# Kernel optimization log

Hardware: AMD Instinct MI355X
Metric: run time of the kernel (lower is better)

Reference implementation:

```python
import jax, jax.numpy as jnp
import numpy as np


def _frac_weights(b_d, k):
    # d = 0.5*sigmoid(b_d), per hidden unit; fractional-differencing coeffs
    # c_j = prod_{i=0}^{j-1} (i - d)/(i + 1), j = 1..k (c_1 = -d).
    # Returned ordered oldest-lag-first to match history buffer ordering.
    d = 0.5 * jax.nn.sigmoid(b_d[0])                      # (H,)
    i = jnp.arange(k, dtype=d.dtype)[:, None]             # (k,1)
    factors = (i - d[None, :]) / (i + 1.0)                # (k,H)
    coeff = jnp.cumprod(factors, axis=0)                  # coeff[j-1] = c_j
    return coeff[::-1]                                    # (k,H)


def setup_inputs() -> dict:
    key = jax.random.key(0)
    T, B, I, H, K, O = 128, 256, 512, 512, 32, 5
    ks = jax.random.split(key, 12)
    s_i = 1.0 / np.sqrt(I)
    s_h = 1.0 / np.sqrt(H)
    return {
        "inputs": jax.random.normal(ks[0], (T, B, I), jnp.float32),
        "length": jax.random.randint(ks[1], (B,), 0, T),
        "b_d": jnp.zeros((1, H), jnp.float32),
        # mLSTM cell (3 gates: input, output, candidate)
        "W_mih": jax.random.normal(ks[2], (3 * H, I), jnp.float32) * s_i,
        "W_mhh": jax.random.normal(ks[3], (3 * H, H), jnp.float32) * s_h,
        "b_mih": jax.random.normal(ks[4], (3 * H,), jnp.float32) * s_h,
        "b_mhh": jax.random.normal(ks[5], (3 * H,), jnp.float32) * s_h,
        # torch.nn.LSTMCell (4 gates: i, f, g, o)
        "W_ih": jax.random.normal(ks[6], (4 * H, H), jnp.float32) * s_h,
        "W_hh": jax.random.normal(ks[7], (4 * H, H), jnp.float32) * s_h,
        "b_ih": jax.random.normal(ks[8], (4 * H,), jnp.float32) * s_h,
        "b_hh": jax.random.normal(ks[9], (4 * H,), jnp.float32) * s_h,
        # hidden2output
        "W_out": jax.random.normal(ks[10], (O, H), jnp.float32) * s_h,
        "b_out": jax.random.normal(ks[11], (O,), jnp.float32) * s_h,
        "k": K,
    }


def reference(inputs, length, b_d, W_mih, W_mhh, b_mih, b_mhh,
              W_ih, W_hh, b_ih, b_hh, W_out, b_out, k):
    T, B, I = inputs.shape
    H = b_d.shape[1]
    wd = _frac_weights(b_d, k)                            # (k,H)

    def step(carry, x_t):
        h1, hist, h2, c2 = carry
        # --- mLSTM fixed-d cell ---
        g = x_t @ W_mih.T + b_mih + h1 @ W_mhh.T + b_mhh  # (B,3H)
        ig, og, gg = jnp.split(g, 3, axis=1)
        i_g, o_g, cand = jax.nn.sigmoid(ig), jax.nn.sigmoid(og), jnp.tanh(gg)
        # fractional-d long-memory filter over last k cell states
        c1 = i_g * cand - jnp.einsum('kh,kbh->bh', wd, hist)
        hist = jnp.concatenate([hist[1:], c1[None]], axis=0)
        h1n = o_g * jnp.tanh(c1)
        # --- standard LSTMCell on top ---
        g2 = h1n @ W_ih.T + b_ih + h2 @ W_hh.T + b_hh     # (B,4H)
        i2, f2, gc2, o2 = jnp.split(g2, 4, axis=1)
        c2n = jax.nn.sigmoid(f2) * c2 + jax.nn.sigmoid(i2) * jnp.tanh(gc2)
        h2n = jnp.tanh(jax.nn.sigmoid(o2) * jnp.tanh(c2n))  # extra tanh as in source
        return (h1n, hist, h2n, c2n), h2n

    z = jnp.zeros((B, H), inputs.dtype)
    init = (z, jnp.zeros((k, B, H), inputs.dtype), z, z)
    _, outs = jax.lax.scan(step, init, inputs)            # (T,B,H)
    sel = outs[length, jnp.arange(B)]                     # (B,H) gather per sample
    logit = sel @ W_out.T + b_out
    return jax.nn.log_softmax(logit, axis=1)
```

## Files before the change

### kernel.cpp

```cpp
#include <hip/hip_runtime.h>
#include <hip/hip_cooperative_groups.h>
#include <cstdint>
#include <cstddef>

typedef __attribute__((ext_vector_type(8))) short short8;
typedef __attribute__((ext_vector_type(4))) float floatx4;

#define T_STEPS 128
#define BATCH   256
#define IDIM    512
#define HDIM    512
#define KHIST   32
#define RDEPTH  16

#define WA_STRIDE 520
#define WB_STRIDE 1032
#define LDS_BYTES 148480

#define FSTR 32
#define POLL_SLEEP 8


__device__ __forceinline__ unsigned short f2bf(float x) {
  union { float f; unsigned u; } v; v.f = x;
  unsigned r = v.u + 0x7fffu + ((v.u >> 16) & 1u);
  return (unsigned short)(r >> 16);
}
__device__ __forceinline__ float bf2f(unsigned short s) {
  union { unsigned u; float f; } v; v.u = ((unsigned)s) << 16; return v.f;
}
__device__ __forceinline__ float sigm(float x) { return 1.0f / (1.0f + __expf(-x)); }
__device__ __forceinline__ float tanh_f(float x) {
  float ax = fabsf(x);
  float e = __expf(-2.0f * ax);
  float t = (1.0f - e) / (1.0f + e);
  return x < 0.0f ? -t : t;
}

__device__ __forceinline__ void llc_issue_16B(const unsigned short* p, short8* r) {
  asm volatile("global_load_dwordx4 %0, %1, off sc0 sc1"
               : "=v"(*r) : "v"(p) : "memory");
}
__device__ __forceinline__ void l2_issue_16B(const unsigned short* p, short8* r) {
  asm volatile("global_load_dwordx4 %0, %1, off sc0"
               : "=v"(*r) : "v"(p) : "memory");
}
__device__ __forceinline__ void llc_store_4rows32(unsigned short* p,
                                                  unsigned short a, unsigned short b,
                                                  unsigned short c, unsigned short d) {
  asm volatile(
    "global_store_short %4, %0, off sc0 sc1\n\t"
    "global_store_short %4, %1, off offset:32 sc0 sc1\n\t"
    "global_store_short %4, %2, off offset:64 sc0 sc1\n\t"
    "global_store_short %4, %3, off offset:96 sc0 sc1"
    :: "v"((unsigned)a), "v"((unsigned)b), "v"((unsigned)c), "v"((unsigned)d), "v"(p)
    : "memory");
}
__device__ __forceinline__ void l2_store_4rows32(unsigned short* p,
                                                 unsigned short a, unsigned short b,
                                                 unsigned short c, unsigned short d) {
  asm volatile(
    "global_store_short %4, %0, off sc0\n\t"
    "global_store_short %4, %1, off offset:32 sc0\n\t"
    "global_store_short %4, %2, off offset:64 sc0\n\t"
    "global_store_short %4, %3, off offset:96 sc0"
    :: "v"((unsigned)a), "v"((unsigned)b), "v"((unsigned)c), "v"((unsigned)d), "v"(p)
    : "memory");
}
__device__ __forceinline__ int flag_ld_llc(const int* p) {
  int v; asm volatile("global_load_dword %0, %1, off sc0 sc1\n\ts_waitcnt vmcnt(0)"
                      : "=v"(v) : "v"(p) : "memory"); return v;
}
__device__ __forceinline__ void flag_st_llc(int* p, int v) {
  asm volatile("global_store_dword %0, %1, off sc0 sc1" :: "v"(p), "v"(v) : "memory");
}
__device__ __forceinline__ void drain_vm() {
  asm volatile("s_waitcnt vmcnt(0)" ::: "memory");
}

#define PREP_BLOCKS 20016
__global__ __launch_bounds__(256) void prep_all(
    const float* __restrict__ x, const float* __restrict__ Wmih, const float* __restrict__ Wmhh,
    const float* __restrict__ Wih, const float* __restrict__ Whh,
    const float* __restrict__ b_d, const float* __restrict__ b_mih, const float* __restrict__ b_mhh,
    const float* __restrict__ b_ih, const float* __restrict__ b_hh,
    unsigned short* __restrict__ Xb, unsigned short* __restrict__ Wmih_b,
    unsigned short* __restrict__ Wmhh_b, unsigned short* __restrict__ W2,
    float* __restrict__ wd2, float* __restrict__ bA, float* __restrict__ bB,
    int* __restrict__ counters) {
  const int blk = blockIdx.x, tid = threadIdx.x;
  if (blk < 16384) {
    int i = blk * 256 + tid;
    float4 v = reinterpret_cast<const float4*>(x)[i];
    ushort4 o; o.x = f2bf(v.x); o.y = f2bf(v.y); o.z = f2bf(v.z); o.w = f2bf(v.w);
    reinterpret_cast<ushort4*>(Xb)[i] = o;
  } else if (blk < 17152) {
    int i = (blk - 16384) * 256 + tid;
    float4 v = reinterpret_cast<const float4*>(Wmih)[i];
    ushort4 o; o.x = f2bf(v.x); o.y = f2bf(v.y); o.z = f2bf(v.z); o.w = f2bf(v.w);
    reinterpret_cast<ushort4*>(Wmih_b)[i] = o;
  } else if (blk < 17920) {
    int i = (blk - 17152) * 256 + tid;
    float4 v = reinterpret_cast<const float4*>(Wmhh)[i];
    ushort4 o; o.x = f2bf(v.x); o.y = f2bf(v.y); o.z = f2bf(v.z); o.w = f2bf(v.w);
    reinterpret_cast<ushort4*>(Wmhh_b)[i] = o;
  } else if (blk < 19968) {
    int i4 = (blk - 17920) * 256 + tid;
    int i = i4 * 4; int n = i >> 10; int k = i & 1023;
    float4 v = (k < 512) ? reinterpret_cast<const float4*>(Wih + n * 512 + k)[0]
                         : reinterpret_cast<const float4*>(Whh + n * 512 + (k - 512))[0];
    ushort4 o; o.x = f2bf(v.x); o.y = f2bf(v.y); o.z = f2bf(v.z); o.w = f2bf(v.w);
    reinterpret_cast<ushort4*>(W2 + i)[0] = o;
  } else if (blk < 19984) {
    int t = (blk - 19968) * 256 + tid;
    if (t < 512) {
      float d = 0.5f * sigm(b_d[t]);
      float c = 1.0f;
      for (int i = 0; i < KHIST; ++i) {
        c *= ((float)i - d) / ((float)i + 1.0f);
        wd2[i * HDIM + t] = c;
      }
    } else if (t < 2048) {
      int n = t - 512;
      bA[n] = b_mih[n] + b_mhh[n];
    } else {
      int n = t - 2048;
      bB[n] = b_ih[n] + b_hh[n];
    }
  } else {
    int i = (blk - 19984) * 256 + tid;
    counters[i] = 0;
  }
}

__global__ __launch_bounds__(256) void gx_gemm_kernel(const unsigned short* __restrict__ Xb,
                                                      const unsigned short* __restrict__ Wb,
                                                      const float* __restrict__ bA,
                                                      unsigned short* __restrict__ GXh) {
  __shared__ unsigned short As[2][128 * 32];
  __shared__ unsigned short Bs[2][128 * 32];
  const int tid = threadIdx.x;
  const int lane = tid & 63;
  const int wv = tid >> 6;
  const int q = lane >> 4, r16 = lane & 15;
  const int wr = wv >> 1, wc = wv & 1;
  const int bid = (int)blockIdx.x;
  const int m0 = (bid & 255) * 128;
  const int n0 = (bid >> 8) * 128;

  const int sr0 = tid >> 2, sc0 = (tid & 3) * 8;
  const int sr1 = (256 + tid) >> 2, sc1 = (tid & 3) * 8;

  floatx4 acc[4][4];
  #pragma unroll
  for (int i = 0; i < 4; ++i)
    #pragma unroll
    for (int j = 0; j < 4; ++j) acc[i][j] = (floatx4){0.f, 0.f, 0.f, 0.f};

  {
    short8 a0 = *(const short8*)(Xb + (size_t)(m0 + sr0) * IDIM + sc0);
    short8 a1 = *(const short8*)(Xb + (size_t)(m0 + sr1) * IDIM + sc1);
    short8 b0 = *(const short8*)(Wb + (size_t)(n0 + sr0) * IDIM + sc0);
    short8 b1 = *(const short8*)(Wb + (size_t)(n0 + sr1) * IDIM + sc1);
    *(short8*)(As[0] + sr0 * 32 + sc0) = a0;
    *(short8*)(As[0] + sr1 * 32 + sc1) = a1;
    *(short8*)(Bs[0] + sr0 * 32 + sc0) = b0;
    *(short8*)(Bs[0] + sr1 * 32 + sc1) = b1;
  }

  for (int t = 0; t < 16; ++t) {
    const int cur = t & 1;
    __syncthreads();
    short8 a0, a1, b0, b1;
    if (t < 15) {
      int k0 = (t + 1) * 32;
      a0 = *(const short8*)(Xb + (size_t)(m0 + sr0) * IDIM + k0 + sc0);
      a1 = *(const short8*)(Xb + (size_t)(m0 + sr1) * IDIM + k0 + sc1);
      b0 = *(const short8*)(Wb + (size_t)(n0 + sr0) * IDIM + k0 + sc0);
      b1 = *(const short8*)(Wb + (size_t)(n0 + sr1) * IDIM + k0 + sc1);
    }
    short8 af[4], bf[4];
    #pragma unroll
    for (int i = 0; i < 4; ++i)
      af[i] = *(const short8*)(As[cur] + (wr * 64 + i * 16 + r16) * 32 + q * 8);
    #pragma unroll
    for (int j = 0; j < 4; ++j)
      bf[j] = *(const short8*)(Bs[cur] + (wc * 64 + j * 16 + r16) * 32 + q * 8);
    #pragma unroll
    for (int i = 0; i < 4; ++i)
      #pragma unroll
      for (int j = 0; j < 4; ++j)
        acc[i][j] = __builtin_amdgcn_mfma_f32_16x16x32_bf16(af[i], bf[j], acc[i][j], 0, 0, 0);
    if (t < 15) {
      *(short8*)(As[cur ^ 1] + sr0 * 32 + sc0) = a0;
      *(short8*)(As[cur ^ 1] + sr1 * 32 + sc1) = a1;
      *(short8*)(Bs[cur ^ 1] + sr0 * 32 + sc0) = b0;
      *(short8*)(Bs[cur ^ 1] + sr1 * 32 + sc1) = b1;
    }
  }

  #pragma unroll
  for (int j = 0; j < 4; ++j) {
    int col = n0 + wc * 64 + j * 16 + r16;
    float bias = bA[col];
    #pragma unroll
    for (int i = 0; i < 4; ++i) {
      #pragma unroll
      for (int jj = 0; jj < 4; ++jj) {
        int row = m0 + wr * 64 + i * 16 + q * 4 + jj;
        GXh[(size_t)row * 1536 + col] = f2bf(acc[i][j][jj] + bias);
      }
    }
  }
}

__global__ __launch_bounds__(512, 1) void recurrent2(
    const unsigned short* __restrict__ GXh,
    const unsigned short* __restrict__ Wmhh,
    const unsigned short* __restrict__ W2,
    const float* __restrict__ bB,
    const float* __restrict__ wd2,
    unsigned short* __restrict__ h1L2,
    unsigned short* __restrict__ h1LLC,
    unsigned short* __restrict__ h2his,
    float* __restrict__ sel,
    const int* __restrict__ length,
    int* __restrict__ counters) {
  extern __shared__ char lds[];
  const int tid = threadIdx.x;
  const int lane = tid & 63;
  const int wv = tid >> 6;
  const int q = lane >> 4, r16 = lane & 15;
  const int xcd = (int)blockIdx.x & 7;
  const int bs = xcd >> 1;
  const bool isA = (xcd & 1) == 0;
  const int hs = (int)blockIdx.x >> 3;
  const int hcol = hs * 16 + r16;
  int* aFlags = counters + bs * 1024;
  int* bFlags = counters + 4096 + bs * 1024;

  if (isA) {
    unsigned short* WA = (unsigned short*)lds;
    unsigned short* HI = (unsigned short*)(lds + 48 * WA_STRIDE * 2);
    for (int idx = tid; idx < 48 * 64; idx += 512) {
      int rowi = idx >> 6, kc = idx & 63;
      int g = rowi >> 4, c = rowi & 15;
      const unsigned short* src = Wmhh + ((size_t)(g * 512 + hs * 16 + c)) * 512 + kc * 8;
      *(short8*)(WA + rowi * WA_STRIDE + kc * 8) = *(const short8*)src;
    }
    for (int idx = tid; idx < 4096; idx += 512)
      ((uint4*)HI)[idx] = (uint4){0, 0, 0, 0};
    float wdr[KHIST];
    #pragma unroll
    for (int l = 0; l < KHIST; ++l) wdr[l] = wd2[l * HDIM + hcol];
    __syncthreads();

    const int mi = wv & 3;
    const int m0 = bs * 64 + mi * 16;
    const int rg = mi * 4 + q;

    for (int s = 0; s < T_STEPS; ++s) {
      unsigned short gu[12];
      if (wv < 4) {
        #pragma unroll
        for (int j = 0; j < 4; ++j) {
          int row = m0 + q * 4 + j;
          size_t gidx = ((size_t)s * BATCH + row) * 1536 + hcol;
          gu[j]     = GXh[gidx];
          gu[4 + j] = GXh[gidx + 512];
          gu[8 + j] = GXh[gidx + 1024];
        }
      }
      if (wv < 4) {
        if (s > 0 && lane < 32) {
          const int* f = aFlags + lane * FSTR;
          while (flag_ld_llc(f) < s) __builtin_amdgcn_s_sleep(POLL_SLEEP);
        }
      } else if (wv == 4) {
        int tgt = s - (RDEPTH - 1);
        if (tgt > 0 && lane < 32) {
          const int* f = bFlags + lane * FSTR;
          while (flag_ld_llc(f) < tgt) __builtin_amdgcn_s_sleep(POLL_SLEEP);
        }
      }
      float c1[4];
      unsigned short h1w[4];
      if (wv < 4) {
        short8 af[16];
        if (s > 0) {
          const unsigned short* ab = h1L2 +
              (((size_t)((s - 1) & 15) * 4 + bs) << 15) +
              (size_t)(mi * 16 + r16) * 16 + (q & 1) * 8 + (q >> 1) * 1024;
          #pragma unroll
          for (int kk = 0; kk < 16; ++kk)
            l2_issue_16B(ab + (size_t)kk * 2048, &af[kk]);
        }
        float f0 = 0.f, f1 = 0.f, f2 = 0.f, f3 = 0.f;
        #pragma unroll
        for (int jj = 1; jj <= KHIST; ++jj) {
          int sl = (s - jj) & (KHIST - 1);
          ushort4 hv = *(const ushort4*)(HI + ((size_t)(sl * 16 + rg) * 16 + r16) * 4);
          float wc = wdr[jj - 1];
          f0 += wc * bf2f(hv.x); f1 += wc * bf2f(hv.y);
          f2 += wc * bf2f(hv.z); f3 += wc * bf2f(hv.w);
        }
        float fj[4] = {f0, f1, f2, f3};
        floatx4 acc[3];
        #pragma unroll
        for (int g = 0; g < 3; ++g) acc[g] = (floatx4){0.f, 0.f, 0.f, 0.f};
        if (s > 0) {
          drain_vm();
          __builtin_amdgcn_sched_barrier(0);
          #pragma unroll
          for (int kk = 0; kk < 16; ++kk) {
            #pragma unroll
            for (int g = 0; g < 3; ++g) {
              short8 b = *(const short8*)(WA + (size_t)(g * 16 + r16) * WA_STRIDE + kk * 32 + q * 8);
              acc[g] = __builtin_amdgcn_mfma_f32_16x16x32_bf16(af[kk], b, acc[g], 0, 0, 0);
            }
          }
        }
        #pragma unroll
        for (int j = 0; j < 4; ++j) {
          float gI = bf2f(gu[j])     + acc[0][j];
          float gO = bf2f(gu[4 + j]) + acc[1][j];
          float gG = bf2f(gu[8 + j]) + acc[2][j];
          float ig = sigm(gI), og = sigm(gO), cd = tanh_f(gG);
          float c1v = ig * cd - fj[j];
          c1[j] = c1v;
          h1w[j] = f2bf(og * tanh_f(c1v));
        }
      }
      __syncthreads();
      if (wv < 4) {
        size_t hoff = (((size_t)(s & 15) * 4 + bs) << 15) + (size_t)hs * 1024 +
                      (size_t)(mi * 16 + q * 4) * 16 + r16;
        l2_store_4rows32(h1L2 + hoff, h1w[0], h1w[1], h1w[2], h1w[3]);
        llc_store_4rows32(h1LLC + hoff, h1w[0], h1w[1], h1w[2], h1w[3]);
        ushort4 hw;
        hw.x = f2bf(c1[0]); hw.y = f2bf(c1[1]); hw.z = f2bf(c1[2]); hw.w = f2bf(c1[3]);
        *(ushort4*)(HI + ((size_t)((s & (KHIST - 1)) * 16 + rg) * 16 + r16) * 4) = hw;
      }
      drain_vm();
      __syncthreads();
      if (tid == 0)
        flag_st_llc(aFlags + hs * FSTR, s + 1);
    }
  } else {
    unsigned short* WB = (unsigned short*)lds;
    float* EX = (float*)(lds + 64 * WB_STRIDE * 2);
    for (int idx = tid; idx < 64 * 128; idx += 512) {
      int rowi = idx >> 7, kc = idx & 127;
      int g = rowi >> 4, c = rowi & 15;
      const unsigned short* src = W2 + ((size_t)(g * 512 + hs * 16 + c)) * 1024 + kc * 8;
      *(short8*)(WB + rowi * WB_STRIDE + kc * 8) = *(const short8*)src;
    }
    const int mi = wv >> 1, kh = wv & 1;
    const int m0 = bs * 64 + mi * 16;
    float c2r[4] = {0.f, 0.f, 0.f, 0.f};
    int lenr[4];
    float bBr[4];
    #pragma unroll
    for (int j = 0; j < 4; ++j) lenr[j] = length[m0 + q * 4 + j];
    #pragma unroll
    for (int g = 0; g < 4; ++g) bBr[g] = bB[g * 512 + hcol];
    __syncthreads();

    for (int t = 0; t < T_STEPS; ++t) {
      if (kh == 0) {
        if (lane < 32) {
          const int* f = aFlags + lane * FSTR;
          while (flag_ld_llc(f) < t + 1) __builtin_amdgcn_s_sleep(POLL_SLEEP);
        }
      } else {
        if (t > 0 && lane < 32) {
          const int* f = bFlags + lane * FSTR;
          while (flag_ld_llc(f) < t) __builtin_amdgcn_s_sleep(POLL_SLEEP);
        }
      }
      floatx4 acc[4];
      #pragma unroll
      for (int g = 0; g < 4; ++g) acc[g] = (floatx4){0.f, 0.f, 0.f, 0.f};
      bool doit = !(kh == 1 && t == 0);
      if (doit) {
        short8 af[16];
        const size_t lrow = (size_t)(mi * 16 + r16) * 16 + (q & 1) * 8 + (q >> 1) * 1024;
        if (kh == 0) {
          const unsigned short* ab = h1LLC + (((size_t)(t & 15) * 4 + bs) << 15) + lrow;
          #pragma unroll
          for (int kk = 0; kk < 16; ++kk)
            llc_issue_16B(ab + (size_t)kk * 2048, &af[kk]);
        } else {
          const unsigned short* ab = h2his + (((size_t)((t - 1) & 15) * 4 + bs) << 15) + lrow;
          #pragma unroll
          for (int kk = 0; kk < 16; ++kk)
            l2_issue_16B(ab + (size_t)kk * 2048, &af[kk]);
        }
        drain_vm();
        __builtin_amdgcn_sched_barrier(0);
        #pragma unroll
        for (int kk = 0; kk < 16; ++kk) {
          #pragma unroll
          for (int g = 0; g < 4; ++g) {
            short8 b = *(const short8*)(WB + (size_t)(g * 16 + r16) * WB_STRIDE + kh * 512 + kk * 32 + q * 8);
            acc[g] = __builtin_amdgcn_mfma_f32_16x16x32_bf16(af[kk], b, acc[g], 0, 0, 0);
          }
        }
      }
      if (kh == 1) {
        #pragma unroll
        for (int g = 0; g < 4; ++g)
          *(floatx4*)(EX + ((size_t)(mi * 4 + g) * 64 + lane) * 4) = acc[g];
      }
      __syncthreads();
      if (kh == 0) {
        #pragma unroll
        for (int g = 0; g < 4; ++g)
          acc[g] += *(const floatx4*)(EX + ((size_t)(mi * 4 + g) * 64 + lane) * 4);
        unsigned short h2w[4];
        #pragma unroll
        for (int j = 0; j < 4; ++j) {
          int row = m0 + q * 4 + j;
          float gi = acc[0][j] + bBr[0];
          float gf = acc[1][j] + bBr[1];
          float gg = acc[2][j] + bBr[2];
          float go = acc[3][j] + bBr[3];
          float c2n = sigm(gf) * c2r[j] + sigm(gi) * tanh_f(gg);
          c2r[j] = c2n;
          float h2n = tanh_f(sigm(go) * tanh_f(c2n));
          h2w[j] = f2bf(h2n);
          if (lenr[j] == t) sel[(size_t)row * 512 + hcol] = h2n;
        }
        size_t hoff = (((size_t)(t & 15) * 4 + bs) << 15) + (size_t)hs * 1024 +
                      (size_t)(mi * 16 + q * 4) * 16 + r16;
        l2_store_4rows32(h2his + hoff, h2w[0], h2w[1], h2w[2], h2w[3]);
      }
      drain_vm();
      __syncthreads();
      if (tid == 0)
        flag_st_llc(bFlags + hs * FSTR, t + 1);
    }
  }
}

__global__ void out_head_kernel(const float* __restrict__ sel, const float* __restrict__ Wout,
                                const float* __restrict__ bout, float* __restrict__ out) {
  int b = blockIdx.x, lane = threadIdx.x;
  float acc[5] = {0.f, 0.f, 0.f, 0.f, 0.f};
  for (int j = lane; j < HDIM; j += 64) {
    float x = sel[(size_t)b * HDIM + j];
    #pragma unroll
    for (int o = 0; o < 5; ++o) acc[o] += x * Wout[o * HDIM + j];
  }
  #pragma unroll
  for (int o = 0; o < 5; ++o)
    for (int off = 32; off > 0; off >>= 1) acc[o] += __shfl_down(acc[o], off);
  if (lane == 0) {
    float v[5]; float m = -1e30f;
    #pragma unroll
    for (int o = 0; o < 5; ++o) { v[o] = acc[o] + bout[o]; m = fmaxf(m, v[o]); }
    float s = 0.f;
    #pragma unroll
    for (int o = 0; o < 5; ++o) s += __expf(v[o] - m);
    float l = logf(s) + m;
    #pragma unroll
    for (int o = 0; o < 5; ++o) out[b * 5 + o] = v[o] - l;
  }
}

extern "C" void kernel_launch(void* const* d_in, const int* in_sizes, int n_in,
                              void* d_out, int out_size, void* d_ws, size_t ws_size,
                              hipStream_t stream) {
  const float* x      = (const float*)d_in[0];
  const int*   length = (const int*)d_in[1];
  const float* b_d    = (const float*)d_in[2];
  const float* W_mih  = (const float*)d_in[3];
  const float* W_mhh  = (const float*)d_in[4];
  const float* b_mih  = (const float*)d_in[5];
  const float* b_mhh  = (const float*)d_in[6];
  const float* W_ih   = (const float*)d_in[7];
  const float* W_hh   = (const float*)d_in[8];
  const float* b_ih   = (const float*)d_in[9];
  const float* b_hh   = (const float*)d_in[10];
  const float* W_out  = (const float*)d_in[11];
  const float* b_out  = (const float*)d_in[12];
  float* out = (float*)d_out;

  char* ws = (char*)d_ws;
  size_t off = 0;
  auto take = [&](size_t bytes) -> char* {
    char* p = ws + off;
    off += (bytes + 255) & ~(size_t)255;
    return p;
  };

  unsigned short* Xb     = (unsigned short*)take((size_t)T_STEPS * BATCH * IDIM * 2);
  unsigned short* Wmih_b = (unsigned short*)take(1536 * 512 * 2);
  unsigned short* Wmhh_b = (unsigned short*)take(1536 * 512 * 2);
  unsigned short* W2_b   = (unsigned short*)take(2048 * 1024 * 2);
  float* bA  = (float*)take(1536 * 4);
  float* bB  = (float*)take(2048 * 4);
  float* wd2 = (float*)take(KHIST * HDIM * 4);
  unsigned short* h1L2  = (unsigned short*)take((size_t)RDEPTH * BATCH * 512 * 2);
  unsigned short* h1LLC = (unsigned short*)take((size_t)RDEPTH * BATCH * 512 * 2);
  unsigned short* h2his = (unsigned short*)take((size_t)RDEPTH * BATCH * 512 * 2);
  float* sel = (float*)take((size_t)BATCH * HDIM * 4);
  int* counters = (int*)take(32768);
  unsigned short* GXh = (unsigned short*)take((size_t)T_STEPS * BATCH * 1536 * 2);
  if (off > ws_size) return;

  prep_all<<<PREP_BLOCKS, 256, 0, stream>>>(x, W_mih, W_mhh, W_ih, W_hh,
                                            b_d, b_mih, b_mhh, b_ih, b_hh,
                                            Xb, Wmih_b, Wmhh_b, W2_b, wd2, bA, bB, counters);
  gx_gemm_kernel<<<3072, 256, 0, stream>>>(Xb, Wmih_b, bA, GXh);

  hipFuncSetAttribute((const void*)recurrent2, hipFuncAttributeMaxDynamicSharedMemorySize, LDS_BYTES);
  void* kargs[] = { (void*)&GXh, (void*)&Wmhh_b, (void*)&W2_b, (void*)&bB, (void*)&wd2,
                    (void*)&h1L2, (void*)&h1LLC, (void*)&h2his, (void*)&sel, (void*)&length,
                    (void*)&counters };
  hipLaunchCooperativeKernel((void*)recurrent2, dim3(256), dim3(512), kargs, LDS_BYTES, stream);

  out_head_kernel<<<BATCH, 64, 0, stream>>>(sel, W_out, b_out, out);
}
```

Before: 1.008 ms.

## Defer LLC publish of h1 by one step and swap LSTM K-half roles

```diff
diff --git a/kernel.cpp b/kernel.cpp
--- a/kernel.cpp
+++ b/kernel.cpp
@@ -258,8 +258,12 @@
     const int mi = wv & 3;
     const int m0 = bs * 64 + mi * 16;
     const int rg = mi * 4 + q;
+    size_t dhoff = 0;
+    unsigned short dh1w[4] = {0, 0, 0, 0};
 
     for (int s = 0; s < T_STEPS; ++s) {
+      if (wv < 4 && s > 0)
+        llc_store_4rows32(h1LLC + dhoff, dh1w[0], dh1w[1], dh1w[2], dh1w[3]);
       unsigned short gu[12];
       if (wv < 4) {
         #pragma unroll
@@ -283,8 +287,6 @@
           while (flag_ld_llc(f) < tgt) __builtin_amdgcn_s_sleep(POLL_SLEEP);
         }
       }
-      float c1[4];
-      unsigned short h1w[4];
       if (wv < 4) {
         short8 af[16];
         if (s > 0) {
@@ -320,6 +322,8 @@
             }
           }
         }
+        float c1[4];
+        unsigned short h1w[4];
         #pragma unroll
         for (int j = 0; j < 4; ++j) {
           float gI = bf2f(gu[j])     + acc[0][j];
@@ -330,13 +334,12 @@
           c1[j] = c1v;
           h1w[j] = f2bf(og * tanh_f(c1v));
         }
-      }
-      __syncthreads();
-      if (wv < 4) {
         size_t hoff = (((size_t)(s & 15) * 4 + bs) << 15) + (size_t)hs * 1024 +
                       (size_t)(mi * 16 + q * 4) * 16 + r16;
         l2_store_4rows32(h1L2 + hoff, h1w[0], h1w[1], h1w[2], h1w[3]);
-        llc_store_4rows32(h1LLC + hoff, h1w[0], h1w[1], h1w[2], h1w[3]);
+        dhoff = hoff;
+        #pragma unroll
+        for (int j = 0; j < 4; ++j) dh1w[j] = h1w[j];
         ushort4 hw;
         hw.x = f2bf(c1[0]); hw.y = f2bf(c1[1]); hw.z = f2bf(c1[2]); hw.w = f2bf(c1[3]);
         *(ushort4*)(HI + ((size_t)((s & (KHIST - 1)) * 16 + rg) * 16 + r16) * 4) = hw;
@@ -346,6 +349,12 @@
       if (tid == 0)
         flag_st_llc(aFlags + hs * FSTR, s + 1);
     }
+    if (wv < 4)
+      llc_store_4rows32(h1LLC + dhoff, dh1w[0], dh1w[1], dh1w[2], dh1w[3]);
+    drain_vm();
+    __syncthreads();
+    if (tid == 0)
+      flag_st_llc(aFlags + hs * FSTR, T_STEPS + 1);
   } else {
     unsigned short* WB = (unsigned short*)lds;
     float* EX = (float*)(lds + 64 * WB_STRIDE * 2);
@@ -367,10 +376,10 @@
     __syncthreads();
 
     for (int t = 0; t < T_STEPS; ++t) {
-      if (kh == 0) {
+      if (kh == 1) {
         if (lane < 32) {
           const int* f = aFlags + lane * FSTR;
-          while (flag_ld_llc(f) < t + 1) __builtin_amdgcn_s_sleep(POLL_SLEEP);
+          while (flag_ld_llc(f) < t + 2) __builtin_amdgcn_s_sleep(POLL_SLEEP);
         }
       } else {
         if (t > 0 && lane < 32) {
@@ -381,36 +390,42 @@
       floatx4 acc[4];
       #pragma unroll
       for (int g = 0; g < 4; ++g) acc[g] = (floatx4){0.f, 0.f, 0.f, 0.f};
-      bool doit = !(kh == 1 && t == 0);
-      if (doit) {
+      const size_t lrow = (size_t)(mi * 16 + r16) * 16 + (q & 1) * 8 + (q >> 1) * 1024;
+      if (kh == 1) {
         short8 af[16];
-        const size_t lrow = (size_t)(mi * 16 + r16) * 16 + (q & 1) * 8 + (q >> 1) * 1024;
-        if (kh == 0) {
-          const unsigned short* ab = h1LLC + (((size_t)(t & 15) * 4 + bs) << 15) + lrow;
-          #pragma unroll
-          for (int kk = 0; kk < 16; ++kk)
-            llc_issue_16B(ab + (size_t)kk * 2048, &af[kk]);
-        } else {
-          const unsigned short* ab = h2his + (((size_t)((t - 1) & 15) * 4 + bs) << 15) + lrow;
-          #pragma unroll
-          for (int kk = 0; kk < 16; ++kk)
-            l2_issue_16B(ab + (size_t)kk * 2048, &af[kk]);
-        }
+        const unsigned short* ab = h1LLC + (((size_t)(t & 15) * 4 + bs) << 15) + lrow;
+        #pragma unroll
+        for (int kk = 0; kk < 16; ++kk)
+          llc_issue_16B(ab + (size_t)kk * 2048, &af[kk]);
         drain_vm();
         __builtin_amdgcn_sched_barrier(0);
         #pragma unroll
         for (int kk = 0; kk < 16; ++kk) {
           #pragma unroll
           for (int g = 0; g < 4; ++g) {
-            short8 b = *(const short8*)(WB + (size_t)(g * 16 + r16) * WB_STRIDE + kh * 512 + kk * 32 + q * 8);
+            short8 b = *(const short8*)(WB + (size_t)(g * 16 + r16) * WB_STRIDE + kk * 32 + q * 8);
             acc[g] = __builtin_amdgcn_mfma_f32_16x16x32_bf16(af[kk], b, acc[g], 0, 0, 0);
           }
         }
-      }
-      if (kh == 1) {
         #pragma unroll
         for (int g = 0; g < 4; ++g)
           *(floatx4*)(EX + ((size_t)(mi * 4 + g) * 64 + lane) * 4) = acc[g];
+      } else if (t > 0) {
+        short8 af[16];
+        const unsigned short* ab = h2his + (((size_t)((t - 1) & 15) * 4 + bs) << 15) + lrow;
+        #pragma unroll
+        for (int kk = 0; kk < 16; ++kk)
+          l2_issue_16B(ab + (size_t)kk * 2048, &af[kk]);
+        drain_vm();
+        __builtin_amdgcn_sched_barrier(0);
+        #pragma unroll
+        for (int kk = 0; kk < 16; ++kk) {
+          #pragma unroll
+          for (int g = 0; g < 4; ++g) {
+            short8 b = *(const short8*)(WB + (size_t)(g * 16 + r16) * WB_STRIDE + 512 + kk * 32 + q * 8);
+            acc[g] = __builtin_amdgcn_mfma_f32_16x16x32_bf16(af[kk], b, acc[g], 0, 0, 0);
+          }
+        }
       }
       __syncthreads();
       if (kh == 0) {
```

Measured after the change: 970.2 us. 3.7% less time.
